# Optimization experiments

Measured on AMD Instinct MI355X. Metric: run time of the kernel, lower is better.

The kernel has to match this reference:

```python
import jax, jax.numpy as jnp
import numpy as np

B, T, C, HS = 4, 4096, 64, 64  # batch, seq (== block_size), num_embedding, head_size


def setup_inputs() -> dict:
    key = jax.random.key(0)
    k1, k2, k3, k4 = jax.random.split(key, 4)
    x = jax.random.normal(k1, (B, T, C), dtype=jnp.float32)
    # nn.Linear(num_embedding, head_size, bias=False) weights, stored as [C, HS]
    # so that projection is x @ W (equivalent to torch's x @ weight.T)
    scale = 1.0 / np.sqrt(C)
    Wq = jax.random.normal(k2, (C, HS), dtype=jnp.float32) * scale
    Wk = jax.random.normal(k3, (C, HS), dtype=jnp.float32) * scale
    Wv = jax.random.normal(k4, (C, HS), dtype=jnp.float32) * scale
    return {"x": x, "Wq": Wq, "Wk": Wk, "Wv": Wv}


def reference(x, Wq, Wk, Wv):
    Bx, Tx, Cx = x.shape
    q = jnp.einsum('btc,ch->bth', x, Wq)
    k = jnp.einsum('btc,ch->bth', x, Wk)
    v = jnp.einsum('btc,ch->bth', x, Wv)
    # NOTE: source multiplies by C**0.5 (quirk of the original code), not 1/sqrt.
    wei = jnp.einsum('bth,bsh->bts', q, k) * (Cx ** 0.5)  # [B,T,T]
    causal = jnp.tril(jnp.ones((Tx, Tx), dtype=bool))
    wei = jnp.where(causal, wei, -jnp.inf)
    wei = jax.nn.softmax(wei, axis=-1)
    return jnp.einsum('bts,bsh->bth', wei, v)
```

## Files before the change

kernel.cpp:

```cpp
#include <hip/hip_runtime.h>
#include <hip/hip_bf16.h>

#define B_ 4
#define T_ 4096

typedef __attribute__((ext_vector_type(8))) short short8;
typedef __attribute__((ext_vector_type(4))) float f32x4;
typedef unsigned short ushort_t;
typedef unsigned int uint32;

__device__ __forceinline__ ushort_t bf16_of(float f) {
    __hip_bfloat16 h = __float2bfloat16(f);
    return __builtin_bit_cast(unsigned short, h);
}

__global__ __launch_bounds__(256) void qkv_proj(
    const float* __restrict__ x, const float* __restrict__ Wq,
    const float* __restrict__ Wk, const float* __restrict__ Wv,
    ushort_t* __restrict__ Qhi, ushort_t* __restrict__ Qlo,
    ushort_t* __restrict__ Khi, ushort_t* __restrict__ Klo,
    ushort_t* __restrict__ Vt)
{
    __shared__ float Ws[3][64][65];
    const int tid = threadIdx.x;
    {
        const float* Wp[3] = {Wq, Wk, Wv};
        for (int mm = 0; mm < 3; ++mm)
            for (int ii = tid; ii < 4096; ii += 256)
                Ws[mm][ii >> 6][ii & 63] = Wp[mm][ii];
    }
    __syncthreads();

    const int w = tid >> 6, lane = tid & 63;
    const int l16 = lane & 15, g = lane >> 4;
    const int R0 = blockIdx.x * 32 + 16 * (w & 1);
    const int h = w >> 1;

    short8 ah[2], al[2];
#pragma unroll
    for (int cc = 0; cc < 2; ++cc) {
        const float* xp = x + (size_t)(R0 + l16) * 64 + cc * 32 + 8 * g;
        float4 v0 = *(const float4*)xp;
        float4 v1 = *(const float4*)(xp + 4);
        float xv[8] = {v0.x, v0.y, v0.z, v0.w, v1.x, v1.y, v1.z, v1.w};
#pragma unroll
        for (int jj = 0; jj < 8; ++jj) {
            __hip_bfloat16 hh = __float2bfloat16(xv[jj]);
            ah[cc][jj] = (short)__builtin_bit_cast(unsigned short, hh);
            al[cc][jj] = (short)bf16_of(xv[jj] - __bfloat162float(hh));
        }
    }

    const float QS = 11.541560327111707f;
#pragma unroll
    for (int u6 = 0; u6 < 6; ++u6) {
        const int u = h * 6 + u6;
        const int mm = u >> 2, ct = u & 3;
        f32x4 d = (f32x4){0.f, 0.f, 0.f, 0.f};
#pragma unroll
        for (int cc = 0; cc < 2; ++cc) {
            short8 bh, bl;
#pragma unroll
            for (int jj = 0; jj < 8; ++jj) {
                float wv = Ws[mm][cc * 32 + 8 * g + jj][ct * 16 + l16];
                __hip_bfloat16 hh = __float2bfloat16(wv);
                bh[jj] = (short)__builtin_bit_cast(unsigned short, hh);
                bl[jj] = (short)bf16_of(wv - __bfloat162float(hh));
            }
            d = __builtin_amdgcn_mfma_f32_16x16x32_bf16(ah[cc], bh, d, 0, 0, 0);
            d = __builtin_amdgcn_mfma_f32_16x16x32_bf16(ah[cc], bl, d, 0, 0, 0);
            d = __builtin_amdgcn_mfma_f32_16x16x32_bf16(al[cc], bh, d, 0, 0, 0);
        }
        const int col = ct * 16 + l16;
        if (mm == 0) {
#pragma unroll
            for (int r = 0; r < 4; ++r) {
                const int R = R0 + 4 * g + r;
                float v = d[r] * QS;
                __hip_bfloat16 hh = __float2bfloat16(v);
                Qhi[(size_t)R * 64 + col] = __builtin_bit_cast(unsigned short, hh);
                Qlo[(size_t)R * 64 + col] = bf16_of(v - __bfloat162float(hh));
            }
        } else if (mm == 1) {
#pragma unroll
            for (int r = 0; r < 4; ++r) {
                const int R = R0 + 4 * g + r;
                float v = d[r];
                __hip_bfloat16 hh = __float2bfloat16(v);
                Khi[(size_t)R * 64 + col] = __builtin_bit_cast(unsigned short, hh);
                Klo[(size_t)R * 64 + col] = bf16_of(v - __bfloat162float(hh));
            }
        } else {
            const int bb = R0 >> 12;
            const int t0 = (R0 & (T_ - 1)) + 4 * g;
            uint32 lo = (uint32)bf16_of(d[0]) | ((uint32)bf16_of(d[1]) << 16);
            uint32 hi = (uint32)bf16_of(d[2]) | ((uint32)bf16_of(d[3]) << 16);
            uint2 pk; pk.x = lo; pk.y = hi;
            *(uint2*)(Vt + ((size_t)(bb * 64 + col)) * T_ + t0) = pk;
        }
    }
}

__global__ __launch_bounds__(256, 2) void flash_attn(
    const ushort_t* __restrict__ Qhi, const ushort_t* __restrict__ Qlo,
    const ushort_t* __restrict__ Khi, const ushort_t* __restrict__ Klo,
    const ushort_t* __restrict__ Vt, float* __restrict__ out)
{
    __shared__ __align__(16) ushort_t Pb[4][2][16][72];
    __shared__ float mrg[2][64][3][26];

    const int tid = threadIdx.x;
    const int p = tid >> 6;
    const int lane = tid & 63;
    const int l16 = lane & 15, g = lane >> 4;

    const int bid = blockIdx.x;
    const int xg = bid & 7;
    const int b = xg & 3;
    const int jj = bid >> 3;
    const int i = (xg >> 2) ? (126 - 2 * jj) : (127 - 2 * jj);
    const int q0 = i * 32;
    const int nkt = (q0 + 32 + 63) >> 6;

    short8 aQh[2][2], aQl[2][2];
#pragma unroll
    for (int su = 0; su < 2; ++su) {
        const size_t qb = ((size_t)(b * T_ + q0 + su * 16 + l16)) * 64;
#pragma unroll
        for (int cc = 0; cc < 2; ++cc) {
            aQh[su][cc] = *(const short8*)(Qhi + qb + cc * 32 + 8 * g);
            aQl[su][cc] = *(const short8*)(Qlo + qb + cc * 32 + 8 * g);
        }
    }

    float m[2][4], lsum[2][4];
    f32x4 acc[2][4];
#pragma unroll
    for (int su = 0; su < 2; ++su)
#pragma unroll
        for (int r = 0; r < 4; ++r) { m[su][r] = -__builtin_inff(); lsum[su][r] = 0.f; }
#pragma unroll
    for (int su = 0; su < 2; ++su)
#pragma unroll
        for (int hs = 0; hs < 4; ++hs) acc[su][hs] = (f32x4){0.f, 0.f, 0.f, 0.f};

    for (int kt = p; kt < nkt; kt += 4) {
        const size_t kb = ((size_t)(b * T_ + kt * 64)) * 64;
        f32x4 sc[2][4];
        __builtin_amdgcn_s_setprio(1);
#pragma unroll
        for (int ks = 0; ks < 4; ++ks) {
            f32x4 a0 = (f32x4){0.f, 0.f, 0.f, 0.f};
            f32x4 a1 = (f32x4){0.f, 0.f, 0.f, 0.f};
#pragma unroll
            for (int cc = 0; cc < 2; ++cc) {
                const size_t ko = kb + ((size_t)(ks * 16 + l16)) * 64 + cc * 32 + 8 * g;
                short8 bh = *(const short8*)(Khi + ko);
                short8 bl = *(const short8*)(Klo + ko);
                a0 = __builtin_amdgcn_mfma_f32_16x16x32_bf16(aQh[0][cc], bh, a0, 0, 0, 0);
                a0 = __builtin_amdgcn_mfma_f32_16x16x32_bf16(aQh[0][cc], bl, a0, 0, 0, 0);
                a0 = __builtin_amdgcn_mfma_f32_16x16x32_bf16(aQl[0][cc], bh, a0, 0, 0, 0);
                a1 = __builtin_amdgcn_mfma_f32_16x16x32_bf16(aQh[1][cc], bh, a1, 0, 0, 0);
                a1 = __builtin_amdgcn_mfma_f32_16x16x32_bf16(aQh[1][cc], bl, a1, 0, 0, 0);
                a1 = __builtin_amdgcn_mfma_f32_16x16x32_bf16(aQl[1][cc], bh, a1, 0, 0, 0);
            }
            sc[0][ks] = a0; sc[1][ks] = a1;
        }
        __builtin_amdgcn_s_setprio(0);
        if (kt == nkt - 1) {
#pragma unroll
            for (int su = 0; su < 2; ++su)
#pragma unroll
                for (int ks = 0; ks < 4; ++ks)
#pragma unroll
                    for (int r = 0; r < 4; ++r) {
                        int key = kt * 64 + ks * 16 + l16;
                        int row = q0 + su * 16 + 4 * g + r;
                        if (key > row) sc[su][ks][r] = -__builtin_inff();
                    }
        }
        float alv[2][4];
#pragma unroll
        for (int su = 0; su < 2; ++su) {
#pragma unroll
            for (int r = 0; r < 4; ++r) {
                float mt = fmaxf(fmaxf(sc[su][0][r], sc[su][1][r]),
                                 fmaxf(sc[su][2][r], sc[su][3][r]));
#pragma unroll
                for (int msk = 1; msk < 16; msk <<= 1) mt = fmaxf(mt, __shfl_xor(mt, msk));
                float mn = fmaxf(m[su][r], mt);
                alv[su][r] = exp2f(m[su][r] - mn);
                m[su][r] = mn;
            }
            float rs[4] = {0.f, 0.f, 0.f, 0.f};
#pragma unroll
            for (int ks = 0; ks < 4; ++ks)
#pragma unroll
                for (int r = 0; r < 4; ++r) {
                    float pv = exp2f(sc[su][ks][r] - m[su][r]);
                    rs[r] += pv;
                    Pb[p][su][4 * g + r][ks * 16 + l16] = bf16_of(pv);
                }
#pragma unroll
            for (int r = 0; r < 4; ++r) {
#pragma unroll
                for (int msk = 1; msk < 16; msk <<= 1) rs[r] += __shfl_xor(rs[r], msk);
                lsum[su][r] = lsum[su][r] * alv[su][r] + rs[r];
            }
#pragma unroll
            for (int hs = 0; hs < 4; ++hs)
#pragma unroll
                for (int r = 0; r < 4; ++r) acc[su][hs][r] *= alv[su][r];
        }
        __builtin_amdgcn_s_setprio(1);
#pragma unroll
        for (int cc = 0; cc < 2; ++cc) {
            short8 ap0 = *(const short8*)&Pb[p][0][l16][cc * 32 + 8 * g];
            short8 ap1 = *(const short8*)&Pb[p][1][l16][cc * 32 + 8 * g];
#pragma unroll
            for (int hs = 0; hs < 4; ++hs) {
                short8 bv = *(const short8*)(Vt + ((size_t)(b * 64 + hs * 16 + l16)) * T_
                                             + kt * 64 + cc * 32 + 8 * g);
                acc[0][hs] = __builtin_amdgcn_mfma_f32_16x16x32_bf16(ap0, bv, acc[0][hs], 0, 0, 0);
                acc[1][hs] = __builtin_amdgcn_mfma_f32_16x16x32_bf16(ap1, bv, acc[1][hs], 0, 0, 0);
            }
        }
        __builtin_amdgcn_s_setprio(0);
    }

    if (p > 0) {
#pragma unroll
        for (int su = 0; su < 2; ++su) {
            float* mp = &mrg[su][lane][p - 1][0];
#pragma unroll
            for (int r = 0; r < 4; ++r) { mp[r] = m[su][r]; mp[4 + r] = lsum[su][r]; }
#pragma unroll
            for (int hs = 0; hs < 4; ++hs)
#pragma unroll
                for (int r = 0; r < 4; ++r) mp[8 + hs * 4 + r] = acc[su][hs][r];
        }
    }
    __syncthreads();
    if (p == 0) {
#pragma unroll
        for (int su = 0; su < 2; ++su) {
#pragma unroll
            for (int r = 0; r < 4; ++r) {
                float mm = m[su][r], ll = lsum[su][r];
                float ac[4];
#pragma unroll
                for (int hs = 0; hs < 4; ++hs) ac[hs] = acc[su][hs][r];
#pragma unroll
                for (int pp = 0; pp < 3; ++pp) {
                    const float* mp = &mrg[su][lane][pp][0];
                    float m1 = mp[r], l1 = mp[4 + r];
                    float mf = fmaxf(mm, m1);
                    float a0 = exp2f(mm - mf);
                    float a1 = exp2f(m1 - mf);
                    ll = ll * a0 + l1 * a1;
#pragma unroll
                    for (int hs = 0; hs < 4; ++hs)
                        ac[hs] = ac[hs] * a0 + mp[8 + hs * 4 + r] * a1;
                    mm = mf;
                }
                float inv = 1.f / ll;
                const size_t ob = ((size_t)(b * T_ + q0 + su * 16 + 4 * g + r)) * 64;
#pragma unroll
                for (int hs = 0; hs < 4; ++hs) out[ob + hs * 16 + l16] = ac[hs] * inv;
            }
        }
    }
}

extern "C" void kernel_launch(void* const* d_in, const int* in_sizes, int n_in,
                              void* d_out, int out_size, void* d_ws, size_t ws_size,
                              hipStream_t stream) {
    const float* x  = (const float*)d_in[0];
    const float* Wq = (const float*)d_in[1];
    const float* Wk = (const float*)d_in[2];
    const float* Wv = (const float*)d_in[3];
    float* out = (float*)d_out;

    const size_t N = (size_t)B_ * T_ * 64;
    ushort_t* Qhi = (ushort_t*)d_ws;
    ushort_t* Qlo = Qhi + N;
    ushort_t* Khi = Qlo + N;
    ushort_t* Klo = Khi + N;
    ushort_t* Vt  = Klo + N;

    qkv_proj<<<512, 256, 0, stream>>>(x, Wq, Wk, Wv, Qhi, Qlo, Khi, Klo, Vt);
    flash_attn<<<512, 256, 0, stream>>>(Qhi, Qlo, Khi, Klo, Vt, out);
}
```

Baseline: 158.0 us.

## Add stream-K split of causal attention work with separate merge kernel

```diff
diff --git a/kernel.cpp b/kernel.cpp
--- a/kernel.cpp
+++ b/kernel.cpp
@@ -3,6 +3,7 @@
 
 #define B_ 4
 #define T_ 4096
+#define UPB 4160
 
 typedef __attribute__((ext_vector_type(8))) short short8;
 typedef __attribute__((ext_vector_type(4))) float f32x4;
@@ -12,6 +13,10 @@
 __device__ __forceinline__ ushort_t bf16_of(float f) {
     __hip_bfloat16 h = __float2bfloat16(f);
     return __builtin_bit_cast(unsigned short, h);
+}
+__device__ __forceinline__ float f_of_bf16(ushort_t u) {
+    uint32 x = ((uint32)u) << 16;
+    return __builtin_bit_cast(float, x);
 }
 
 __global__ __launch_bounds__(256) void qkv_proj(
@@ -101,6 +106,220 @@
     }
 }
 
+__global__ __launch_bounds__(256, 3) void flash_sk(
+    const ushort_t* __restrict__ Qhi, const ushort_t* __restrict__ Qlo,
+    const ushort_t* __restrict__ Khi, const ushort_t* __restrict__ Klo,
+    const ushort_t* __restrict__ Vt,
+    ushort_t* __restrict__ PACC, float* __restrict__ PML,
+    const int S, const int SLOTS)
+{
+    __shared__ __align__(16) ushort_t Pb[4][2][16][72];
+
+    const int tid = threadIdx.x;
+    const int wv = tid >> 6;
+    const int lane = tid & 63;
+    const int l16 = lane & 15, g = lane >> 4;
+
+    const int W = blockIdx.x * 4 + wv;
+    int u = (65 * W) / S;
+    const int uEnd = (65 * (W + 1)) / S;
+
+    while (u < uEnd) {
+        const int b = u / UPB;
+        const int r = u - b * UPB;
+        int t = (int)sqrtf((float)r);
+        while ((t + 1) * (t + 1) <= r) ++t;
+        while (t * t > r) --t;
+        int i, kt0;
+        if (r < t * t + t) { i = 2 * t - 1; kt0 = r - t * t; }
+        else               { i = 2 * t;     kt0 = r - t * t - t; }
+        const int nkt = (i >> 1) + 1;
+        const int q0 = i * 32;
+        const int rem = nkt - kt0;
+        const int avail = uEnd - u;
+        const int run = (rem < avail) ? rem : avail;
+
+        short8 aQh[2][2], aQl[2][2];
+#pragma unroll
+        for (int su = 0; su < 2; ++su) {
+            const size_t qb = ((size_t)(b * T_ + q0 + su * 16 + l16)) * 64;
+#pragma unroll
+            for (int cc = 0; cc < 2; ++cc) {
+                aQh[su][cc] = *(const short8*)(Qhi + qb + cc * 32 + 8 * g);
+                aQl[su][cc] = *(const short8*)(Qlo + qb + cc * 32 + 8 * g);
+            }
+        }
+
+        float m[2][4], lsum[2][4];
+        f32x4 acc[2][4];
+#pragma unroll
+        for (int su = 0; su < 2; ++su)
+#pragma unroll
+            for (int rr = 0; rr < 4; ++rr) { m[su][rr] = -__builtin_inff(); lsum[su][rr] = 0.f; }
+#pragma unroll
+        for (int su = 0; su < 2; ++su)
+#pragma unroll
+            for (int hs = 0; hs < 4; ++hs) acc[su][hs] = (f32x4){0.f, 0.f, 0.f, 0.f};
+
+        for (int e = 0; e < run; ++e) {
+            const int kt = kt0 + e;
+            const size_t kb = ((size_t)(b * T_ + kt * 64)) * 64;
+            f32x4 sc[2][4];
+            __builtin_amdgcn_s_setprio(1);
+#pragma unroll
+            for (int ks = 0; ks < 4; ++ks) {
+                f32x4 a0 = (f32x4){0.f, 0.f, 0.f, 0.f};
+                f32x4 a1 = (f32x4){0.f, 0.f, 0.f, 0.f};
+#pragma unroll
+                for (int cc = 0; cc < 2; ++cc) {
+                    const size_t ko = kb + ((size_t)(ks * 16 + l16)) * 64 + cc * 32 + 8 * g;
+                    short8 bh = *(const short8*)(Khi + ko);
+                    short8 bl = *(const short8*)(Klo + ko);
+                    a0 = __builtin_amdgcn_mfma_f32_16x16x32_bf16(aQh[0][cc], bh, a0, 0, 0, 0);
+                    a0 = __builtin_amdgcn_mfma_f32_16x16x32_bf16(aQh[0][cc], bl, a0, 0, 0, 0);
+                    a0 = __builtin_amdgcn_mfma_f32_16x16x32_bf16(aQl[0][cc], bh, a0, 0, 0, 0);
+                    a1 = __builtin_amdgcn_mfma_f32_16x16x32_bf16(aQh[1][cc], bh, a1, 0, 0, 0);
+                    a1 = __builtin_amdgcn_mfma_f32_16x16x32_bf16(aQh[1][cc], bl, a1, 0, 0, 0);
+                    a1 = __builtin_amdgcn_mfma_f32_16x16x32_bf16(aQl[1][cc], bh, a1, 0, 0, 0);
+                }
+                sc[0][ks] = a0; sc[1][ks] = a1;
+            }
+            __builtin_amdgcn_s_setprio(0);
+            if (kt == nkt - 1) {
+#pragma unroll
+                for (int su = 0; su < 2; ++su)
+#pragma unroll
+                    for (int ks = 0; ks < 4; ++ks)
+#pragma unroll
+                        for (int rr = 0; rr < 4; ++rr) {
+                            int key = kt * 64 + ks * 16 + l16;
+                            int row = q0 + su * 16 + 4 * g + rr;
+                            if (key > row) sc[su][ks][rr] = -__builtin_inff();
+                        }
+            }
+            float alv[2][4];
+#pragma unroll
+            for (int su = 0; su < 2; ++su) {
+#pragma unroll
+                for (int rr = 0; rr < 4; ++rr) {
+                    float mt = fmaxf(fmaxf(sc[su][0][rr], sc[su][1][rr]),
+                                     fmaxf(sc[su][2][rr], sc[su][3][rr]));
+#pragma unroll
+                    for (int msk = 1; msk < 16; msk <<= 1) mt = fmaxf(mt, __shfl_xor(mt, msk));
+                    float mn = fmaxf(m[su][rr], mt);
+                    alv[su][rr] = exp2f(m[su][rr] - mn);
+                    m[su][rr] = mn;
+                }
+                float rs[4] = {0.f, 0.f, 0.f, 0.f};
+#pragma unroll
+                for (int ks = 0; ks < 4; ++ks)
+#pragma unroll
+                    for (int rr = 0; rr < 4; ++rr) {
+                        float pv = exp2f(sc[su][ks][rr] - m[su][rr]);
+                        rs[rr] += pv;
+                        Pb[wv][su][4 * g + rr][ks * 16 + l16] = bf16_of(pv);
+                    }
+#pragma unroll
+                for (int rr = 0; rr < 4; ++rr) {
+#pragma unroll
+                    for (int msk = 1; msk < 16; msk <<= 1) rs[rr] += __shfl_xor(rs[rr], msk);
+                    lsum[su][rr] = lsum[su][rr] * alv[su][rr] + rs[rr];
+                }
+#pragma unroll
+                for (int hs = 0; hs < 4; ++hs)
+#pragma unroll
+                    for (int rr = 0; rr < 4; ++rr) acc[su][hs][rr] *= alv[su][rr];
+            }
+            __builtin_amdgcn_s_setprio(1);
+#pragma unroll
+            for (int cc = 0; cc < 2; ++cc) {
+                short8 ap0 = *(const short8*)&Pb[wv][0][l16][cc * 32 + 8 * g];
+                short8 ap1 = *(const short8*)&Pb[wv][1][l16][cc * 32 + 8 * g];
+#pragma unroll
+                for (int hs = 0; hs < 4; ++hs) {
+                    short8 bv = *(const short8*)(Vt + ((size_t)(b * 64 + hs * 16 + l16)) * T_
+                                                 + kt * 64 + cc * 32 + 8 * g);
+                    acc[0][hs] = __builtin_amdgcn_mfma_f32_16x16x32_bf16(ap0, bv, acc[0][hs], 0, 0, 0);
+                    acc[1][hs] = __builtin_amdgcn_mfma_f32_16x16x32_bf16(ap1, bv, acc[1][hs], 0, 0, 0);
+                }
+            }
+            __builtin_amdgcn_s_setprio(0);
+        }
+
+        {
+            const int mh = i >> 1;
+            const int Si = (i & 1) ? (mh + 1) * (mh + 1) : mh * (mh + 1);
+            const int A = b * UPB + Si;
+            const int Wf = (S * A + S - 1) / 65;
+            const int slot = W - Wf;
+            const int Tid = b * 128 + i;
+            ushort_t* pa = PACC + ((size_t)(Tid * SLOTS + slot)) * 2048;
+            float* pm = PML + ((size_t)(Tid * SLOTS + slot)) * 64;
+#pragma unroll
+            for (int su = 0; su < 2; ++su)
+#pragma unroll
+                for (int hs = 0; hs < 4; ++hs)
+#pragma unroll
+                    for (int rr = 0; rr < 4; ++rr)
+                        pa[(su * 16 + 4 * g + rr) * 64 + hs * 16 + l16] = bf16_of(acc[su][hs][rr]);
+            if (l16 == 0) {
+#pragma unroll
+                for (int su = 0; su < 2; ++su)
+#pragma unroll
+                    for (int rr = 0; rr < 4; ++rr) {
+                        const int row = su * 16 + 4 * g + rr;
+                        pm[row * 2] = m[su][rr];
+                        pm[row * 2 + 1] = lsum[su][rr];
+                    }
+            }
+        }
+        u += run;
+    }
+}
+
+__global__ __launch_bounds__(256) void merge_k(
+    const ushort_t* __restrict__ PACC, const float* __restrict__ PML,
+    float* __restrict__ out, const int S, const int SLOTS)
+{
+    const int tid = threadIdx.x;
+    const int Tid = blockIdx.x;
+    const int b = Tid >> 7, i = Tid & 127;
+    const int nkt = (i >> 1) + 1;
+    const int mh = i >> 1;
+    const int Si = (i & 1) ? (mh + 1) * (mh + 1) : mh * (mh + 1);
+    const int A = b * UPB + Si;
+    const int Wf = (S * A + S - 1) / 65;
+    const int Wl = (S * (A + nkt - 1) + S - 1) / 65;
+    const int n = Wl - Wf + 1;
+    const int row = tid >> 3;
+    const int c0 = (tid & 7) * 8;
+
+    float mm = -__builtin_inff(), ll = 0.f;
+    float ac[8];
+#pragma unroll
+    for (int k2 = 0; k2 < 8; ++k2) ac[k2] = 0.f;
+
+    for (int p = 0; p < n; ++p) {
+        const float* pm = PML + ((size_t)(Tid * SLOTS + p)) * 64 + row * 2;
+        float m1 = pm[0], l1 = pm[1];
+        short8 pv = *(const short8*)(PACC + ((size_t)(Tid * SLOTS + p)) * 2048 + row * 64 + c0);
+        float mf = fmaxf(mm, m1);
+        float a0 = exp2f(mm - mf), a1 = exp2f(m1 - mf);
+        ll = ll * a0 + l1 * a1;
+#pragma unroll
+        for (int k2 = 0; k2 < 8; ++k2)
+            ac[k2] = ac[k2] * a0 + f_of_bf16((ushort_t)pv[k2]) * a1;
+        mm = mf;
+    }
+    float inv = 1.f / ll;
+    float* op = out + ((size_t)(b * T_ + i * 32 + row)) * 64 + c0;
+    float4 o0, o1;
+    o0.x = ac[0] * inv; o0.y = ac[1] * inv; o0.z = ac[2] * inv; o0.w = ac[3] * inv;
+    o1.x = ac[4] * inv; o1.y = ac[5] * inv; o1.z = ac[6] * inv; o1.w = ac[7] * inv;
+    *(float4*)op = o0;
+    *(float4*)(op + 4) = o1;
+}
+
 __global__ __launch_bounds__(256, 2) void flash_attn(
     const ushort_t* __restrict__ Qhi, const ushort_t* __restrict__ Qlo,
     const ushort_t* __restrict__ Khi, const ushort_t* __restrict__ Klo,
@@ -138,7 +357,7 @@
 #pragma unroll
     for (int su = 0; su < 2; ++su)
 #pragma unroll
-        for (int r = 0; r < 4; ++r) { m[su][r] = -__builtin_inff(); lsum[su][r] = 0.f; }
+        for (int rr = 0; rr < 4; ++rr) { m[su][rr] = -__builtin_inff(); lsum[su][rr] = 0.f; }
 #pragma unroll
     for (int su = 0; su < 2; ++su)
 #pragma unroll
@@ -173,44 +392,44 @@
 #pragma unroll
                 for (int ks = 0; ks < 4; ++ks)
 #pragma unroll
-                    for (int r = 0; r < 4; ++r) {
+                    for (int rr = 0; rr < 4; ++rr) {
                         int key = kt * 64 + ks * 16 + l16;
-                        int row = q0 + su * 16 + 4 * g + r;
-                        if (key > row) sc[su][ks][r] = -__builtin_inff();
+                        int row = q0 + su * 16 + 4 * g + rr;
+                        if (key > row) sc[su][ks][rr] = -__builtin_inff();
                     }
         }
         float alv[2][4];
 #pragma unroll
         for (int su = 0; su < 2; ++su) {
 #pragma unroll
-            for (int r = 0; r < 4; ++r) {
-                float mt = fmaxf(fmaxf(sc[su][0][r], sc[su][1][r]),
-                                 fmaxf(sc[su][2][r], sc[su][3][r]));
+            for (int rr = 0; rr < 4; ++rr) {
+                float mt = fmaxf(fmaxf(sc[su][0][rr], sc[su][1][rr]),
+                                 fmaxf(sc[su][2][rr], sc[su][3][rr]));
 #pragma unroll
                 for (int msk = 1; msk < 16; msk <<= 1) mt = fmaxf(mt, __shfl_xor(mt, msk));
-                float mn = fmaxf(m[su][r], mt);
-                alv[su][r] = exp2f(m[su][r] - mn);
-                m[su][r] = mn;
+                float mn = fmaxf(m[su][rr], mt);
+                alv[su][rr] = exp2f(m[su][rr] - mn);
+                m[su][rr] = mn;
             }
             float rs[4] = {0.f, 0.f, 0.f, 0.f};
 #pragma unroll
             for (int ks = 0; ks < 4; ++ks)
 #pragma unroll
-                for (int r = 0; r < 4; ++r) {
-                    float pv = exp2f(sc[su][ks][r] - m[su][r]);
-                    rs[r] += pv;
-                    Pb[p][su][4 * g + r][ks * 16 + l16] = bf16_of(pv);
+                for (int rr = 0; rr < 4; ++rr) {
+                    float pv = exp2f(sc[su][ks][rr] - m[su][rr]);
+                    rs[rr] += pv;
+                    Pb[p][su][4 * g + rr][ks * 16 + l16] = bf16_of(pv);
                 }
 #pragma unroll
-            for (int r = 0; r < 4; ++r) {
-#pragma unroll
-                for (int msk = 1; msk < 16; msk <<= 1) rs[r] += __shfl_xor(rs[r], msk);
-                lsum[su][r] = lsum[su][r] * alv[su][r] + rs[r];
+            for (int rr = 0; rr < 4; ++rr) {
+#pragma unroll
+                for (int msk = 1; msk < 16; msk <<= 1) rs[rr] += __shfl_xor(rs[rr], msk);
+                lsum[su][rr] = lsum[su][rr] * alv[su][rr] + rs[rr];
             }
 #pragma unroll
             for (int hs = 0; hs < 4; ++hs)
 #pragma unroll
-                for (int r = 0; r < 4; ++r) acc[su][hs][r] *= alv[su][r];
+                for (int rr = 0; rr < 4; ++rr) acc[su][hs][rr] *= alv[su][rr];
         }
         __builtin_amdgcn_s_setprio(1);
 #pragma unroll
@@ -233,11 +452,11 @@
         for (int su = 0; su < 2; ++su) {
             float* mp = &mrg[su][lane][p - 1][0];
 #pragma unroll
-            for (int r = 0; r < 4; ++r) { mp[r] = m[su][r]; mp[4 + r] = lsum[su][r]; }
+            for (int rr = 0; rr < 4; ++rr) { mp[rr] = m[su][rr]; mp[4 + rr] = lsum[su][rr]; }
 #pragma unroll
             for (int hs = 0; hs < 4; ++hs)
 #pragma unroll
-                for (int r = 0; r < 4; ++r) mp[8 + hs * 4 + r] = acc[su][hs][r];
+                for (int rr = 0; rr < 4; ++rr) mp[8 + hs * 4 + rr] = acc[su][hs][rr];
         }
     }
     __syncthreads();
@@ -245,26 +464,26 @@
 #pragma unroll
         for (int su = 0; su < 2; ++su) {
 #pragma unroll
-            for (int r = 0; r < 4; ++r) {
-                float mm = m[su][r], ll = lsum[su][r];
+            for (int rr = 0; rr < 4; ++rr) {
+                float mm = m[su][rr], ll = lsum[su][rr];
                 float ac[4];
 #pragma unroll
-                for (int hs = 0; hs < 4; ++hs) ac[hs] = acc[su][hs][r];
+                for (int hs = 0; hs < 4; ++hs) ac[hs] = acc[su][hs][rr];
 #pragma unroll
                 for (int pp = 0; pp < 3; ++pp) {
                     const float* mp = &mrg[su][lane][pp][0];
-                    float m1 = mp[r], l1 = mp[4 + r];
+                    float m1 = mp[rr], l1 = mp[4 + rr];
                     float mf = fmaxf(mm, m1);
                     float a0 = exp2f(mm - mf);
                     float a1 = exp2f(m1 - mf);
                     ll = ll * a0 + l1 * a1;
 #pragma unroll
                     for (int hs = 0; hs < 4; ++hs)
-                        ac[hs] = ac[hs] * a0 + mp[8 + hs * 4 + r] * a1;
+                        ac[hs] = ac[hs] * a0 + mp[8 + hs * 4 + rr] * a1;
                     mm = mf;
                 }
                 float inv = 1.f / ll;
-                const size_t ob = ((size_t)(b * T_ + q0 + su * 16 + 4 * g + r)) * 64;
+                const size_t ob = ((size_t)(b * T_ + q0 + su * 16 + 4 * g + rr)) * 64;
 #pragma unroll
                 for (int hs = 0; hs < 4; ++hs) out[ob + hs * 16 + l16] = ac[hs] * inv;
             }
@@ -287,7 +506,25 @@
     ushort_t* Khi = Qlo + N;
     ushort_t* Klo = Khi + N;
     ushort_t* Vt  = Klo + N;
+    ushort_t* PACC = Vt + N;
+
+    const size_t base = 5 * N * sizeof(ushort_t);
+    const size_t need12 = base + (size_t)512 * 13 * (2048 * 2 + 256);
+    const size_t need8  = base + (size_t)512 * 9  * (2048 * 2 + 256);
 
     qkv_proj<<<512, 256, 0, stream>>>(x, Wq, Wk, Wv, Qhi, Qlo, Khi, Klo, Vt);
-    flash_attn<<<512, 256, 0, stream>>>(Qhi, Qlo, Khi, Klo, Vt, out);
-}
+
+    if (ws_size >= need12) {
+        const int S = 12, SLOTS = 13;
+        float* PML = (float*)(PACC + (size_t)512 * SLOTS * 2048);
+        flash_sk<<<768, 256, 0, stream>>>(Qhi, Qlo, Khi, Klo, Vt, PACC, PML, S, SLOTS);
+        merge_k<<<512, 256, 0, stream>>>(PACC, PML, out, S, SLOTS);
+    } else if (ws_size >= need8) {
+        const int S = 8, SLOTS = 9;
+        float* PML = (float*)(PACC + (size_t)512 * SLOTS * 2048);
+        flash_sk<<<512, 256, 0, stream>>>(Qhi, Qlo, Khi, Klo, Vt, PACC, PML, S, SLOTS);
+        merge_k<<<512, 256, 0, stream>>>(PACC, PML, out, S, SLOTS);
+    } else {
+        flash_attn<<<512, 256, 0, stream>>>(Qhi, Qlo, Khi, Klo, Vt, out);
+    }
+}
```

Measured after the change: 149.9 us. 5.1% less time.
